# Kernel optimization log

Measured on AMD Instinct MI355X. Metric: run time of the kernel, lower is better.

Reference implementation:

```python
import jax, jax.numpy as jnp
import numpy as np


def setup_inputs() -> dict:
    key = jax.random.key(0)
    k1, k2 = jax.random.split(key)
    N, P, SMK, L = 256, 64, 2048, 32
    inp = jax.random.normal(k1, (N, P, SMK, 2), dtype=jnp.float32)
    # channel taps; in the original these are randn scaled by sqrt(power/2)
    cof = jax.random.normal(k2, (N, P, L, 2), dtype=jnp.float32) * 0.1
    return {"input": inp, "cof": cof, "M": 64}


def reference(input, cof, M):
    # input: (N, P, SMK, 2) real/imag stacked; cof: (N, P, L, 2)
    N, P, SMK, _ = input.shape
    L = cof.shape[2]
    sig = (input[..., 0] + 1j * input[..., 1]).reshape(N * P, SMK)   # complex64
    h = (cof[..., 0] + 1j * cof[..., 1]).reshape(N * P, L)
    # torch path: conv1d with time-reversed taps and padding=L-1 == FULL linear
    # convolution; four real convs == one complex conv.
    out_c = jax.vmap(lambda s, k: jnp.convolve(s, k, mode="full"))(sig, h)  # (N*P, SMK+L-1)
    output = jnp.stack([out_c.real, out_c.imag], axis=-1).reshape(N, P, SMK + L - 1, 2)
    # H_t = FFT of zero-padded taps along the tap axis (length M)
    cof_zp = jnp.pad(cof, ((0, 0), (0, 0), (0, M - L), (0, 0)))
    Hc = jnp.fft.fft(cof_zp[..., 0] + 1j * cof_zp[..., 1], axis=-1)  # (N, P, M)
    H_t = jnp.stack([Hc.real, Hc.imag], axis=-1)                      # (N, P, M, 2)
    return output, H_t
```

## Files before the change

### kernel.cpp

```cpp
#include <hip/hip_runtime.h>
#include <math.h>

#define SMK    2048
#define TAPS   32
#define OUTLEN (SMK + TAPS - 1)
#define PAD    32
#define SLOTS  (PAD + SMK + PAD)
#define MDFT   64
#define NF4    1040

__device__ __forceinline__ int swz(int p) { return p ^ ((p >> 4) & 15); }
__device__ __forceinline__ int swz4(int s) { return s ^ ((s >> 3) & 7); }

__device__ __forceinline__ float rfl(float x) {
    return __int_as_float(__builtin_amdgcn_readfirstlane(__float_as_int(x)));
}

__global__ __launch_bounds__(256, 4)
void conv_kernel(const float* __restrict__ input,
                 const float* __restrict__ cof,
                 float* __restrict__ out0,
                 float* __restrict__ out1)
{
    __shared__ float2 s_sig[SLOTS];
    __shared__ float4 s_out[NF4];
    __shared__ float2 s_tap[TAPS];
    __shared__ float2 s_tw[MDFT];

    const int tid = threadIdx.x;
    const int row = blockIdx.x;

    const float4* gin = (const float4*)(input + (size_t)row * SMK * 2);
    #pragma unroll
    for (int k = 0; k < 4; ++k) {
        float4 v = gin[tid + 256 * k];
        int i0 = PAD + 2 * (tid + 256 * k);
        s_sig[swz(i0)]     = make_float2(v.x, v.y);
        s_sig[swz(i0 + 1)] = make_float2(v.z, v.w);
    }
    if (tid < PAD) {
        s_sig[swz(tid)] = make_float2(0.f, 0.f);
    } else if (tid < 2 * PAD) {
        s_sig[swz(SMK + tid)] = make_float2(0.f, 0.f);
    }
    if (tid < TAPS) {
        const float2* ct = (const float2*)(cof + (size_t)row * TAPS * 2);
        s_tap[tid] = ct[tid];
    }
    if (tid >= 64 && tid < 128) {
        int j = tid - 64;
        float sv, cv;
        __sincosf(-2.0f * (float)M_PI * (float)j / (float)MDFT, &sv, &cv);
        s_tw[j] = make_float2(cv, sv);
    }
    __syncthreads();

    float hre[TAPS], him[TAPS];
    #pragma unroll
    for (int l = 0; l < TAPS; ++l) {
        float2 h = s_tap[l];
        hre[l] = rfl(h.x);
        him[l] = rfl(h.y);
    }

    const int t0 = tid * 8;

    float2 win[39];
    #pragma unroll
    for (int m = 0; m < 39; ++m) win[m] = s_sig[swz(t0 + 1 + m)];

    float2 acc[8];
    #pragma unroll
    for (int k = 0; k < 8; ++k) acc[k] = make_float2(0.f, 0.f);

    #pragma unroll
    for (int l = 0; l < TAPS; ++l) {
        const float hr = hre[l];
        const float hi = him[l];
        #pragma unroll
        for (int k = 0; k < 8; ++k) {
            float2 s = win[k + 31 - l];
            acc[k].x = fmaf(s.x, hr, fmaf(-s.y, hi, acc[k].x));
            acc[k].y = fmaf(s.x, hi, fmaf( s.y, hr, acc[k].y));
        }
    }

    #pragma unroll
    for (int k = 0; k < 4; ++k) {
        float4 v = make_float4(acc[2 * k].x, acc[2 * k].y,
                               acc[2 * k + 1].x, acc[2 * k + 1].y);
        s_out[swz4(4 * tid + k)] = v;
    }

    if (tid < OUTLEN - SMK) {
        const int t = SMK + tid;
        float2 a = make_float2(0.f, 0.f);
        #pragma unroll
        for (int l = 0; l < TAPS; ++l) {
            float2 s = s_sig[swz(t - l + PAD)];
            a.x = fmaf(s.x, hre[l], fmaf(-s.y, him[l], a.x));
            a.y = fmaf(s.x, him[l], fmaf( s.y, hre[l], a.y));
        }
        float2* so2 = (float2*)s_out;
        so2[swz4(t >> 1) * 2 + (t & 1)] = a;
    }

    if (tid < MDFT) {
        const int k = tid;
        float2 a = make_float2(0.f, 0.f);
        #pragma unroll
        for (int l = 0; l < TAPS; ++l) {
            float2 w = s_tw[(k * l) & (MDFT - 1)];
            a.x = fmaf(w.x, hre[l], fmaf(-w.y, him[l], a.x));
            a.y = fmaf(w.y, hre[l], fmaf( w.x, him[l], a.y));
        }
        ((float2*)out1)[(size_t)row * MDFT + k] = a;
    }

    __syncthreads();

    const float2* so2 = (const float2*)s_out;
    float2* go2 = (float2*)(out0 + (size_t)row * OUTLEN * 2);
    #pragma unroll
    for (int it = 0; it < 8; ++it) {
        int s2 = tid + 256 * it;
        go2[s2] = so2[swz4(s2 >> 1) * 2 + (s2 & 1)];
    }
    {
        int s2 = tid + 2048;
        if (s2 < OUTLEN)
            go2[s2] = so2[swz4(s2 >> 1) * 2 + (s2 & 1)];
    }
}

extern "C" void kernel_launch(void* const* d_in, const int* in_sizes, int n_in,
                              void* d_out, int out_size, void* d_ws, size_t ws_size,
                              hipStream_t stream)
{
    const float* input = (const float*)d_in[0];
    const float* cof   = (const float*)d_in[1];

    const int NP = in_sizes[0] / (SMK * 2);

    float* out0 = (float*)d_out;
    float* out1 = out0 + (size_t)NP * OUTLEN * 2;

    conv_kernel<<<NP, 256, 0, stream>>>(input, cof, out0, out1);
}
```

Baseline: 154.8 us.

## Restructure conv into per-thread output pairs with direct global stores

Each thread now computes two adjacent outputs per iteration over four strided chunks, reading its window straight from unswizzled LDS as float4s. Results go directly to global memory, so the output staging buffer, swizzle math and second barrier are gone. Taps are loaded from global memory straight into scalar registers, and the DFT and tail work move to different wavefronts so they run in parallel. The cost is much less register-level data reuse (a 17-float4 window for two outputs instead of 39 float2 for eight), so LDS traffic per FMA rises, and the global stores become less coalesced 8-byte writes.

```diff
diff --git a/kernel.cpp b/kernel.cpp
--- a/kernel.cpp
+++ b/kernel.cpp
@@ -7,10 +7,6 @@
 #define PAD    32
 #define SLOTS  (PAD + SMK + PAD)
 #define MDFT   64
-#define NF4    1040
-
-__device__ __forceinline__ int swz(int p) { return p ^ ((p >> 4) & 15); }
-__device__ __forceinline__ int swz4(int s) { return s ^ ((s >> 3) & 7); }
 
 __device__ __forceinline__ float rfl(float x) {
     return __int_as_float(__builtin_amdgcn_readfirstlane(__float_as_int(x)));
@@ -23,29 +19,32 @@
                  float* __restrict__ out1)
 {
     __shared__ float2 s_sig[SLOTS];
-    __shared__ float4 s_out[NF4];
-    __shared__ float2 s_tap[TAPS];
     __shared__ float2 s_tw[MDFT];
 
     const int tid = threadIdx.x;
     const int row = blockIdx.x;
 
+    const float2* __restrict__ ct = (const float2*)(cof + (size_t)row * (TAPS * 2));
+    float hre[TAPS], him[TAPS];
+    #pragma unroll
+    for (int l = 0; l < TAPS; ++l) {
+        float2 tv = ct[l];
+        hre[l] = rfl(tv.x);
+        him[l] = rfl(tv.y);
+    }
+
     const float4* gin = (const float4*)(input + (size_t)row * SMK * 2);
+    float4* s4 = (float4*)s_sig;
+    float4 stg[4];
     #pragma unroll
-    for (int k = 0; k < 4; ++k) {
-        float4 v = gin[tid + 256 * k];
-        int i0 = PAD + 2 * (tid + 256 * k);
-        s_sig[swz(i0)]     = make_float2(v.x, v.y);
-        s_sig[swz(i0 + 1)] = make_float2(v.z, v.w);
-    }
+    for (int k = 0; k < 4; ++k) stg[k] = gin[tid + 256 * k];
+    #pragma unroll
+    for (int k = 0; k < 4; ++k) s4[(PAD / 2) + tid + 256 * k] = stg[k];
+
     if (tid < PAD) {
-        s_sig[swz(tid)] = make_float2(0.f, 0.f);
+        s_sig[tid] = make_float2(0.f, 0.f);
     } else if (tid < 2 * PAD) {
-        s_sig[swz(SMK + tid)] = make_float2(0.f, 0.f);
-    }
-    if (tid < TAPS) {
-        const float2* ct = (const float2*)(cof + (size_t)row * TAPS * 2);
-        s_tap[tid] = ct[tid];
+        s_sig[SMK + tid] = make_float2(0.f, 0.f);
     }
     if (tid >= 64 && tid < 128) {
         int j = tid - 64;
@@ -55,81 +54,61 @@
     }
     __syncthreads();
 
-    float hre[TAPS], him[TAPS];
-    #pragma unroll
-    for (int l = 0; l < TAPS; ++l) {
-        float2 h = s_tap[l];
-        hre[l] = rfl(h.x);
-        him[l] = rfl(h.y);
+    float2* go2 = (float2*)(out0 + (size_t)row * OUTLEN * 2);
+
+    #pragma unroll 1
+    for (int j = 0; j < 4; ++j) {
+        const int t0 = 2 * tid + 512 * j;
+        const float4* base = s4 + (t0 >> 1);
+        float4 w4[17];
+        #pragma unroll
+        for (int i = 0; i < 17; ++i) w4[i] = base[i];
+
+        float a0x = 0.f, a0y = 0.f, a1x = 0.f, a1y = 0.f;
+        #pragma unroll
+        for (int l = 0; l < TAPS; ++l) {
+            const float hr = hre[l];
+            const float hi = him[l];
+            {
+                const int m = 32 - l;
+                const float sx = (m & 1) ? w4[m >> 1].z : w4[m >> 1].x;
+                const float sy = (m & 1) ? w4[m >> 1].w : w4[m >> 1].y;
+                a0x = fmaf(sx, hr, fmaf(-sy, hi, a0x));
+                a0y = fmaf(sx, hi, fmaf( sy, hr, a0y));
+            }
+            {
+                const int m = 33 - l;
+                const float sx = (m & 1) ? w4[m >> 1].z : w4[m >> 1].x;
+                const float sy = (m & 1) ? w4[m >> 1].w : w4[m >> 1].y;
+                a1x = fmaf(sx, hr, fmaf(-sy, hi, a1x));
+                a1y = fmaf(sx, hi, fmaf( sy, hr, a1y));
+            }
+        }
+        go2[t0]     = make_float2(a0x, a0y);
+        go2[t0 + 1] = make_float2(a1x, a1y);
     }
 
-    const int t0 = tid * 8;
-
-    float2 win[39];
-    #pragma unroll
-    for (int m = 0; m < 39; ++m) win[m] = s_sig[swz(t0 + 1 + m)];
-
-    float2 acc[8];
-    #pragma unroll
-    for (int k = 0; k < 8; ++k) acc[k] = make_float2(0.f, 0.f);
-
-    #pragma unroll
-    for (int l = 0; l < TAPS; ++l) {
-        const float hr = hre[l];
-        const float hi = him[l];
-        #pragma unroll
-        for (int k = 0; k < 8; ++k) {
-            float2 s = win[k + 31 - l];
-            acc[k].x = fmaf(s.x, hr, fmaf(-s.y, hi, acc[k].x));
-            acc[k].y = fmaf(s.x, hi, fmaf( s.y, hr, acc[k].y));
-        }
-    }
-
-    #pragma unroll
-    for (int k = 0; k < 4; ++k) {
-        float4 v = make_float4(acc[2 * k].x, acc[2 * k].y,
-                               acc[2 * k + 1].x, acc[2 * k + 1].y);
-        s_out[swz4(4 * tid + k)] = v;
-    }
-
-    if (tid < OUTLEN - SMK) {
-        const int t = SMK + tid;
-        float2 a = make_float2(0.f, 0.f);
-        #pragma unroll
-        for (int l = 0; l < TAPS; ++l) {
-            float2 s = s_sig[swz(t - l + PAD)];
-            a.x = fmaf(s.x, hre[l], fmaf(-s.y, him[l], a.x));
-            a.y = fmaf(s.x, him[l], fmaf( s.y, hre[l], a.y));
-        }
-        float2* so2 = (float2*)s_out;
-        so2[swz4(t >> 1) * 2 + (t & 1)] = a;
-    }
-
-    if (tid < MDFT) {
-        const int k = tid;
-        float2 a = make_float2(0.f, 0.f);
+    if (tid >= 64 && tid < 128) {
+        const int k = tid - 64;
+        float ax = 0.f, ay = 0.f;
         #pragma unroll
         for (int l = 0; l < TAPS; ++l) {
             float2 w = s_tw[(k * l) & (MDFT - 1)];
-            a.x = fmaf(w.x, hre[l], fmaf(-w.y, him[l], a.x));
-            a.y = fmaf(w.y, hre[l], fmaf( w.x, him[l], a.y));
+            ax = fmaf(w.x, hre[l], fmaf(-w.y, him[l], ax));
+            ay = fmaf(w.y, hre[l], fmaf( w.x, him[l], ay));
         }
-        ((float2*)out1)[(size_t)row * MDFT + k] = a;
+        ((float2*)out1)[(size_t)row * MDFT + k] = make_float2(ax, ay);
     }
-
-    __syncthreads();
-
-    const float2* so2 = (const float2*)s_out;
-    float2* go2 = (float2*)(out0 + (size_t)row * OUTLEN * 2);
-    #pragma unroll
-    for (int it = 0; it < 8; ++it) {
-        int s2 = tid + 256 * it;
-        go2[s2] = so2[swz4(s2 >> 1) * 2 + (s2 & 1)];
-    }
-    {
-        int s2 = tid + 2048;
-        if (s2 < OUTLEN)
-            go2[s2] = so2[swz4(s2 >> 1) * 2 + (s2 & 1)];
+    else if (tid >= 128 && tid < 128 + (OUTLEN - SMK)) {
+        const int t = SMK + (tid - 128);
+        float ax = 0.f, ay = 0.f;
+        #pragma unroll
+        for (int l = 0; l < TAPS; ++l) {
+            float2 s = s_sig[PAD + t - l];
+            ax = fmaf(s.x, hre[l], fmaf(-s.y, him[l], ax));
+            ay = fmaf(s.x, him[l], fmaf( s.y, hre[l], ay));
+        }
+        go2[t] = make_float2(ax, ay);
     }
 }
 
```

Measured after the change: 237.4 us. 1.53x slower.

## Use packed FMA for complex conv, drop LDS output staging and tap smem

Applied to the files above, without the earlier changes.

Rewrites the complex multiply-accumulate as two packed v2f FMAs per sample (split real/imag accumulators, combined at the end), which lets the compiler emit packed FP32 FMA instructions. Output is now written directly from registers to global memory instead of being staged through shared memory, which removes the second barrier and the LDS buffer. Taps are read straight from global into scalar registers. The tail outputs and the DFT are moved onto different thread ranges so they run in parallel. The price is strided, less coalesced global stores: each thread writes 8 consecutive float2 values.

```diff
diff --git a/kernel.cpp b/kernel.cpp
--- a/kernel.cpp
+++ b/kernel.cpp
@@ -7,30 +7,29 @@
 #define PAD    32
 #define SLOTS  (PAD + SMK + PAD)
 #define MDFT   64
-#define NF4    1040
+
+typedef float v2f __attribute__((ext_vector_type(2)));
 
 __device__ __forceinline__ int swz(int p) { return p ^ ((p >> 4) & 15); }
-__device__ __forceinline__ int swz4(int s) { return s ^ ((s >> 3) & 7); }
 
 __device__ __forceinline__ float rfl(float x) {
     return __int_as_float(__builtin_amdgcn_readfirstlane(__float_as_int(x)));
 }
 
-__global__ __launch_bounds__(256, 4)
+__global__ __launch_bounds__(256)
+__attribute__((amdgpu_waves_per_eu(4, 4)))
 void conv_kernel(const float* __restrict__ input,
                  const float* __restrict__ cof,
                  float* __restrict__ out0,
                  float* __restrict__ out1)
 {
     __shared__ float2 s_sig[SLOTS];
-    __shared__ float4 s_out[NF4];
-    __shared__ float2 s_tap[TAPS];
     __shared__ float2 s_tw[MDFT];
 
     const int tid = threadIdx.x;
     const int row = blockIdx.x;
 
-    const float4* gin = (const float4*)(input + (size_t)row * SMK * 2);
+    const float4* gin = (const float4*)(input + (size_t)row * (SMK * 2));
     #pragma unroll
     for (int k = 0; k < 4; ++k) {
         float4 v = gin[tid + 256 * k];
@@ -43,25 +42,22 @@
     } else if (tid < 2 * PAD) {
         s_sig[swz(SMK + tid)] = make_float2(0.f, 0.f);
     }
-    if (tid < TAPS) {
-        const float2* ct = (const float2*)(cof + (size_t)row * TAPS * 2);
-        s_tap[tid] = ct[tid];
-    }
     if (tid >= 64 && tid < 128) {
         int j = tid - 64;
         float sv, cv;
         __sincosf(-2.0f * (float)M_PI * (float)j / (float)MDFT, &sv, &cv);
         s_tw[j] = make_float2(cv, sv);
     }
-    __syncthreads();
 
+    const float2* __restrict__ ct = (const float2*)(cof + (size_t)row * (TAPS * 2));
     float hre[TAPS], him[TAPS];
     #pragma unroll
     for (int l = 0; l < TAPS; ++l) {
-        float2 h = s_tap[l];
-        hre[l] = rfl(h.x);
-        him[l] = rfl(h.y);
+        float2 tv = ct[l];
+        hre[l] = rfl(tv.x);
+        him[l] = rfl(tv.y);
     }
+    __syncthreads();
 
     const int t0 = tid * 8;
 
@@ -69,67 +65,50 @@
     #pragma unroll
     for (int m = 0; m < 39; ++m) win[m] = s_sig[swz(t0 + 1 + m)];
 
-    float2 acc[8];
+    v2f accA[8], accB[8];
     #pragma unroll
-    for (int k = 0; k < 8; ++k) acc[k] = make_float2(0.f, 0.f);
+    for (int k = 0; k < 8; ++k) { accA[k] = (v2f)(0.f); accB[k] = (v2f)(0.f); }
 
     #pragma unroll
     for (int l = 0; l < TAPS; ++l) {
-        const float hr = hre[l];
-        const float hi = him[l];
+        const v2f hv = { hre[l], him[l] };
         #pragma unroll
         for (int k = 0; k < 8; ++k) {
-            float2 s = win[k + 31 - l];
-            acc[k].x = fmaf(s.x, hr, fmaf(-s.y, hi, acc[k].x));
-            acc[k].y = fmaf(s.x, hi, fmaf( s.y, hr, acc[k].y));
+            const float2 s = win[k + 31 - l];
+            accA[k] = __builtin_elementwise_fma((v2f){ s.x, s.x }, hv, accA[k]);
+            accB[k] = __builtin_elementwise_fma((v2f){ s.y, s.y }, hv, accB[k]);
         }
     }
 
+    float2* go2 = (float2*)(out0 + (size_t)row * (OUTLEN * 2));
     #pragma unroll
-    for (int k = 0; k < 4; ++k) {
-        float4 v = make_float4(acc[2 * k].x, acc[2 * k].y,
-                               acc[2 * k + 1].x, acc[2 * k + 1].y);
-        s_out[swz4(4 * tid + k)] = v;
-    }
+    for (int k = 0; k < 8; ++k)
+        go2[t0 + k] = make_float2(accA[k].x - accB[k].y, accA[k].y + accB[k].x);
 
-    if (tid < OUTLEN - SMK) {
-        const int t = SMK + tid;
-        float2 a = make_float2(0.f, 0.f);
+    if (tid < MDFT) {
+        const int kk = tid;
+        v2f aA = (v2f)(0.f), aB = (v2f)(0.f);
         #pragma unroll
         for (int l = 0; l < TAPS; ++l) {
-            float2 s = s_sig[swz(t - l + PAD)];
-            a.x = fmaf(s.x, hre[l], fmaf(-s.y, him[l], a.x));
-            a.y = fmaf(s.x, him[l], fmaf( s.y, hre[l], a.y));
+            const v2f hv = { hre[l], him[l] };
+            float2 w = s_tw[(kk * l) & (MDFT - 1)];
+            aA = __builtin_elementwise_fma((v2f){ w.x, w.x }, hv, aA);
+            aB = __builtin_elementwise_fma((v2f){ w.y, w.y }, hv, aB);
         }
-        float2* so2 = (float2*)s_out;
-        so2[swz4(t >> 1) * 2 + (t & 1)] = a;
+        ((float2*)out1)[(size_t)row * MDFT + kk] =
+            make_float2(aA.x - aB.y, aA.y + aB.x);
     }
-
-    if (tid < MDFT) {
-        const int k = tid;
-        float2 a = make_float2(0.f, 0.f);
+    else if (tid >= 128 && tid < 128 + (OUTLEN - SMK)) {
+        const int t = SMK + (tid - 128);
+        v2f aA = (v2f)(0.f), aB = (v2f)(0.f);
         #pragma unroll
         for (int l = 0; l < TAPS; ++l) {
-            float2 w = s_tw[(k * l) & (MDFT - 1)];
-            a.x = fmaf(w.x, hre[l], fmaf(-w.y, him[l], a.x));
-            a.y = fmaf(w.y, hre[l], fmaf( w.x, him[l], a.y));
+            const v2f hv = { hre[l], him[l] };
+            float2 s = s_sig[swz(PAD + t - l)];
+            aA = __builtin_elementwise_fma((v2f){ s.x, s.x }, hv, aA);
+            aB = __builtin_elementwise_fma((v2f){ s.y, s.y }, hv, aB);
         }
-        ((float2*)out1)[(size_t)row * MDFT + k] = a;
-    }
-
-    __syncthreads();
-
-    const float2* so2 = (const float2*)s_out;
-    float2* go2 = (float2*)(out0 + (size_t)row * OUTLEN * 2);
-    #pragma unroll
-    for (int it = 0; it < 8; ++it) {
-        int s2 = tid + 256 * it;
-        go2[s2] = so2[swz4(s2 >> 1) * 2 + (s2 & 1)];
-    }
-    {
-        int s2 = tid + 2048;
-        if (s2 < OUTLEN)
-            go2[s2] = so2[swz4(s2 >> 1) * 2 + (s2 & 1)];
+        go2[t] = make_float2(aA.x - aB.y, aA.y + aB.x);
     }
 }
 
```

Result: faster. 146.4 us (-5.5%).
